# Kernel tuning notes

Hardware: AMD Instinct MI355X
Metric: run time of the kernel (lower is better)

The kernel has to match this reference:

```python
import jax, jax.numpy as jnp
import numpy as np

MOMENTUM = 0.9


def setup_inputs() -> dict:
    key = jax.random.key(0)
    k1, k2, k3, k4 = jax.random.split(key, 4)
    B, D, C = 524288, 256, 1000
    x = jax.random.normal(k1, (B, D), dtype=jnp.float32)
    l = jax.random.randint(k2, (B,), 0, C, dtype=jnp.int64)
    center_img = jax.random.normal(k3, (C, D), dtype=jnp.float32)
    center_skt = jax.random.normal(k4, (C, D), dtype=jnp.float32)
    return {"x": x, "l": l, "center_img": center_img, "center_skt": center_skt}


def reference(x, l, center_img, center_skt):
    # Faithful vectorized version of CenterAlignment.forward (modality='img').
    # The per-sample Python scatter-add loop -> segment_sum over fixed num_classes;
    # torch.unique's data-dependent class set -> boolean 'present' mask.
    C = center_img.shape[0]
    counts = jax.ops.segment_sum(jnp.ones(x.shape[0], dtype=x.dtype), l, num_segments=C)  # [C]
    sums = jax.ops.segment_sum(x, l, num_segments=C)                                      # [C, D]
    present = counts > 0
    mean = sums / jnp.maximum(counts, 1.0)[:, None]  # per-class mean (safe div for absent classes)
    # momentum update + L2 renormalization, only for classes present in the batch
    upd = center_img * MOMENTUM + mean * (1.0 - MOMENTUM)
    upd = upd / jnp.linalg.norm(upd, axis=1, keepdims=True)
    new_img = jnp.where(present[:, None], upd, center_img)
    # align_loss with alpha=2: mean over present classes of ||c_img - c_skt||^2
    diff = new_img - center_skt
    sq = jnp.sum(diff * diff, axis=1)  # [C]
    n_present = jnp.maximum(jnp.sum(present.astype(x.dtype)), 1.0)
    loss = jnp.sum(jnp.where(present, sq, 0.0)) / n_present
    return loss
```

## Files before the change

kernel.cpp:

```cpp
#include <hip/hip_runtime.h>

#define MAXC    1000
#define DSUB    16
#define LSTR    17
#define THREADS 1024
#define NCHUNK  32
#define FIXS    1048576.0f
#define INVFIXS (1.0f / 1048576.0f)

__global__ __launch_bounds__(THREADS, 8) void scatter_kernel(
    const float* __restrict__ x, const int* __restrict__ l,
    int* __restrict__ sums_i, int* __restrict__ cnt_i,
    int B, int D, int C, int chunk)
{
    __shared__ int lsum[MAXC * LSTR];
    __shared__ int lcnt[MAXC];

    for (int i = threadIdx.x; i < MAXC * LSTR; i += THREADS) lsum[i] = 0;
    for (int i = threadIdx.x; i < MAXC; i += THREADS) lcnt[i] = 0;
    __syncthreads();

    const bool doCount = (blockIdx.y == 0);
    const int dbase = blockIdx.y * DSUB;
    const int q    = threadIdx.x & 3;
    const int srel = threadIdx.x >> 2;
    const int STEP = THREADS >> 2;
    const int DV   = D >> 2;
    const int qb   = (dbase >> 2) + q;

    const float4* __restrict__ x4 = (const float4*)x;

    const int s0 = blockIdx.x * chunk;
    const int s1 = min(B, s0 + chunk);

#define ACC4(cc, vv)                                                   \
    {                                                                  \
        const int b_ = (cc) * LSTR + (q << 2);                         \
        atomicAdd(&lsum[b_ + 0], __float2int_rn((vv).x * FIXS));       \
        atomicAdd(&lsum[b_ + 1], __float2int_rn((vv).y * FIXS));       \
        atomicAdd(&lsum[b_ + 2], __float2int_rn((vv).z * FIXS));       \
        atomicAdd(&lsum[b_ + 3], __float2int_rn((vv).w * FIXS));       \
    }

    int s = s0 + srel;
    if (s + 3 * STEP < s1) {
        int c0 = l[s];
        int c1 = l[s + STEP];
        int c2 = l[s + 2 * STEP];
        int c3 = l[s + 3 * STEP];
        float4 v0 = x4[(size_t)s * DV + qb];
        float4 v1 = x4[(size_t)(s + STEP) * DV + qb];
        float4 v2 = x4[(size_t)(s + 2 * STEP) * DV + qb];
        float4 v3 = x4[(size_t)(s + 3 * STEP) * DV + qb];
        int sn = s + 4 * STEP;
        for (; sn + 3 * STEP < s1; sn += 4 * STEP) {
            int n0 = l[sn];
            int n1 = l[sn + STEP];
            int n2 = l[sn + 2 * STEP];
            int n3 = l[sn + 3 * STEP];
            float4 w0 = x4[(size_t)sn * DV + qb];
            float4 w1 = x4[(size_t)(sn + STEP) * DV + qb];
            float4 w2 = x4[(size_t)(sn + 2 * STEP) * DV + qb];
            float4 w3 = x4[(size_t)(sn + 3 * STEP) * DV + qb];
            ACC4(c0, v0); ACC4(c1, v1); ACC4(c2, v2); ACC4(c3, v3);
            if (doCount && q == 0) {
                atomicAdd(&lcnt[c0], 1);
                atomicAdd(&lcnt[c1], 1);
                atomicAdd(&lcnt[c2], 1);
                atomicAdd(&lcnt[c3], 1);
            }
            c0 = n0; c1 = n1; c2 = n2; c3 = n3;
            v0 = w0; v1 = w1; v2 = w2; v3 = w3;
        }
        ACC4(c0, v0); ACC4(c1, v1); ACC4(c2, v2); ACC4(c3, v3);
        if (doCount && q == 0) {
            atomicAdd(&lcnt[c0], 1);
            atomicAdd(&lcnt[c1], 1);
            atomicAdd(&lcnt[c2], 1);
            atomicAdd(&lcnt[c3], 1);
        }
        s = sn;
    }
    for (; s < s1; s += STEP) {
        int c = l[s];
        float4 v = x4[(size_t)s * DV + qb];
        ACC4(c, v);
        if (doCount && q == 0) atomicAdd(&lcnt[c], 1);
    }
    __syncthreads();

    for (int i = threadIdx.x; i < C * DSUB; i += THREADS) {
        const int c = i >> 4, d = i & (DSUB - 1);
        const int v = lsum[c * LSTR + d];
        if (v) atomicAdd(&sums_i[(size_t)c * D + dbase + d], v);
    }
    if (doCount)
        for (int i = threadIdx.x; i < C; i += THREADS) {
            const int v = lcnt[i];
            if (v) atomicAdd(&cnt_i[i], v);
        }
#undef ACC4
}

__device__ __forceinline__ float block_reduce_sum_256(float v, float* sbuf) {
    #pragma unroll
    for (int o = 32; o > 0; o >>= 1) v += __shfl_down(v, o, 64);
    __syncthreads();
    if ((threadIdx.x & 63) == 0) sbuf[threadIdx.x >> 6] = v;
    __syncthreads();
    return sbuf[0] + sbuf[1] + sbuf[2] + sbuf[3];
}

__global__ __launch_bounds__(256) void update_kernel(
    const int* __restrict__ sums_i, const int* __restrict__ cnt_i,
    const float* __restrict__ cimg, const float* __restrict__ cskt,
    float* __restrict__ sq_out, float* __restrict__ pres_out, int C, int D)
{
    __shared__ float sbuf[4];
    __shared__ float cshare;
    const int c = blockIdx.x;
    const int t = threadIdx.x;

    const float ssum = (float)sums_i[(size_t)c * D + t] * INVFIXS;
    if (t == 0) cshare = (float)cnt_i[c];
    __syncthreads();
    const float cnt = cshare;

    const bool present = cnt > 0.5f;
    const size_t idx = (size_t)c * D + t;
    const float ci = cimg[idx];
    const float cs = cskt[idx];
    const float mean = ssum / fmaxf(cnt, 1.f);
    const float upd = ci * 0.9f + mean * 0.1f;
    const float n2 = block_reduce_sum_256(upd * upd, sbuf);
    const float inv = 1.0f / sqrtf(n2);
    const float newv = present ? upd * inv : ci;
    const float df = newv - cs;
    const float sq = block_reduce_sum_256(df * df, sbuf);
    if (t == 0) {
        sq_out[c]   = present ? sq : 0.f;
        pres_out[c] = present ? 1.f : 0.f;
    }
}

__global__ __launch_bounds__(256) void finalize_kernel(
    const float* __restrict__ sq, const float* __restrict__ pres,
    float* __restrict__ out, int C)
{
    __shared__ float sbuf[4];
    float ls = 0.f, np = 0.f;
    for (int i = threadIdx.x; i < C; i += 256) {
        ls += sq[i];
        np += pres[i];
    }
    ls = block_reduce_sum_256(ls, sbuf);
    np = block_reduce_sum_256(np, sbuf);
    if (threadIdx.x == 0) out[0] = ls / fmaxf(np, 1.f);
}

extern "C" void kernel_launch(void* const* d_in, const int* in_sizes, int n_in,
                              void* d_out, int out_size, void* d_ws, size_t ws_size,
                              hipStream_t stream) {
    const float* x    = (const float*)d_in[0];
    const int*   l    = (const int*)d_in[1];
    const float* cimg = (const float*)d_in[2];
    const float* cskt = (const float*)d_in[3];

    const int B = in_sizes[1];
    const int D = in_sizes[0] / B;
    const int C = in_sizes[2] / D;

    int*   sums_i = (int*)d_ws;
    int*   cnt_i  = sums_i + (size_t)C * D;
    float* sq     = (float*)(cnt_i + C);
    float* pres   = sq + C;

    hipMemsetAsync(d_ws, 0, sizeof(int) * ((size_t)C * D + C), stream);

    const int chunk = (B + NCHUNK - 1) / NCHUNK;
    dim3 grid(NCHUNK, D / DSUB);

    scatter_kernel<<<grid, THREADS, 0, stream>>>(x, l, sums_i, cnt_i, B, D, C, chunk);
    update_kernel<<<C, 256, 0, stream>>>(sums_i, cnt_i, cimg, cskt, sq, pres, C, D);
    finalize_kernel<<<1, 256, 0, stream>>>(sq, pres, (float*)d_out, C);
}
```

Measured before the change: 142.4 us.

## Replace shared-memory atomic scatter with counting-sort by class then segmented sums

Replaces the per-block LDS-atomic scatter with a pipeline: histogram of labels, prefix scan, a permutation build that groups row indices by class, then a wave-per-span segmented sum that reads rows in sorted order and flushes register accumulators to global memory with atomics only at class boundaries. This is meant to remove the heavy LDS atomic traffic. In exchange it adds three extra launches, global atomics on per-class cursors, and gathered (non-contiguous) row reads of x. The build step also makes the within-class order nondeterministic, though the integer fixed-point sums stay exact.

Measured after the change: 168.7 us. 1.18x slower.

```diff
diff --git a/kernel.cpp b/kernel.cpp
--- a/kernel.cpp
+++ b/kernel.cpp
@@ -1,105 +1,109 @@
 #include <hip/hip_runtime.h>
 
-#define MAXC    1000
-#define DSUB    16
-#define LSTR    17
-#define THREADS 1024
-#define NCHUNK  32
+#define CMAX    1000
+#define CPAD    64
 #define FIXS    1048576.0f
 #define INVFIXS (1.0f / 1048576.0f)
 
-__global__ __launch_bounds__(THREADS, 8) void scatter_kernel(
-    const float* __restrict__ x, const int* __restrict__ l,
-    int* __restrict__ sums_i, int* __restrict__ cnt_i,
-    int B, int D, int C, int chunk)
+__global__ __launch_bounds__(256) void hist_kernel(
+    const int* __restrict__ l, int* __restrict__ tot, int B)
 {
-    __shared__ int lsum[MAXC * LSTR];
-    __shared__ int lcnt[MAXC];
+    __shared__ int h[CMAX];
+    for (int i = threadIdx.x; i < CMAX; i += 256) h[i] = 0;
+    __syncthreads();
+    const int per  = (B + gridDim.x - 1) / gridDim.x;
+    const int base = blockIdx.x * per;
+    const int end  = min(B, base + per);
+    for (int i = base + threadIdx.x; i < end; i += 256)
+        atomicAdd(&h[l[i]], 1);
+    __syncthreads();
+    for (int i = threadIdx.x; i < CMAX; i += 256) {
+        const int v = h[i];
+        if (v) atomicAdd(&tot[i], v);
+    }
+}
 
-    for (int i = threadIdx.x; i < MAXC * LSTR; i += THREADS) lsum[i] = 0;
-    for (int i = threadIdx.x; i < MAXC; i += THREADS) lcnt[i] = 0;
+__global__ __launch_bounds__(1024) void scan_kernel(
+    const int* __restrict__ tot, int* __restrict__ cursor,
+    int* __restrict__ cnt_i, int C)
+{
+    __shared__ int s[1024];
+    const int t = threadIdx.x;
+    const int v = (t < C) ? tot[t] : 0;
+    s[t] = v;
+    if (t < C) cnt_i[t] = v;
+    for (int off = 1; off < 1024; off <<= 1) {
+        __syncthreads();
+        const int u = (t >= off) ? s[t - off] : 0;
+        __syncthreads();
+        s[t] += u;
+    }
     __syncthreads();
+    if (t < C) cursor[t * CPAD] = s[t] - v;
+}
 
-    const bool doCount = (blockIdx.y == 0);
-    const int dbase = blockIdx.y * DSUB;
-    const int q    = threadIdx.x & 3;
-    const int srel = threadIdx.x >> 2;
-    const int STEP = THREADS >> 2;
-    const int DV   = D >> 2;
-    const int qb   = (dbase >> 2) + q;
+__global__ __launch_bounds__(256) void build_kernel(
+    const int* __restrict__ l, int* __restrict__ cursor,
+    int* __restrict__ perm, int* __restrict__ lsorted, int B)
+{
+    const int per  = (B + gridDim.x - 1) / gridDim.x;
+    const int base = blockIdx.x * per;
+    const int end  = min(B, base + per);
+    for (int i = base + threadIdx.x; i < end; i += 256) {
+        const int c   = l[i];
+        const int pos = atomicAdd(&cursor[c * CPAD], 1);
+        perm[pos]    = i;
+        lsorted[pos] = c;
+    }
+}
 
+#define SPAN 64
+__global__ __launch_bounds__(256) void segsum_kernel(
+    const float* __restrict__ x, const int* __restrict__ perm,
+    const int* __restrict__ lsorted, int* __restrict__ sums_i, int B, int D)
+{
+    const int lane = threadIdx.x & 63;
+    const int wid  = (int)((blockIdx.x * blockDim.x + threadIdx.x) >> 6);
+    const int p0 = wid * SPAN;
+    if (p0 >= B) return;
+    const int p1 = min(B, p0 + SPAN);
+    const int DV = D >> 2;
     const float4* __restrict__ x4 = (const float4*)x;
 
-    const int s0 = blockIdx.x * chunk;
-    const int s1 = min(B, s0 + chunk);
+    int cur = lsorted[p0];
+    int ax = 0, ay = 0, az = 0, aw = 0;
 
-#define ACC4(cc, vv)                                                   \
-    {                                                                  \
-        const int b_ = (cc) * LSTR + (q << 2);                         \
-        atomicAdd(&lsum[b_ + 0], __float2int_rn((vv).x * FIXS));       \
-        atomicAdd(&lsum[b_ + 1], __float2int_rn((vv).y * FIXS));       \
-        atomicAdd(&lsum[b_ + 2], __float2int_rn((vv).z * FIXS));       \
-        atomicAdd(&lsum[b_ + 3], __float2int_rn((vv).w * FIXS));       \
+    int    c_n   = cur;
+    int    idx_n = perm[p0];
+    float4 v_n   = x4[(size_t)idx_n * DV + lane];
+
+    for (int p = p0; p < p1; ++p) {
+        const float4 v = v_n;
+        const int    c = c_n;
+        if (p + 1 < p1) {
+            const int idx2 = perm[p + 1];
+            c_n = lsorted[p + 1];
+            v_n = x4[(size_t)idx2 * DV + lane];
+        }
+        if (c != cur) {
+            int* dst = sums_i + (size_t)cur * D + (lane << 2);
+            atomicAdd(dst + 0, ax);
+            atomicAdd(dst + 1, ay);
+            atomicAdd(dst + 2, az);
+            atomicAdd(dst + 3, aw);
+            ax = ay = az = aw = 0;
+            cur = c;
+        }
+        ax += __float2int_rn(v.x * FIXS);
+        ay += __float2int_rn(v.y * FIXS);
+        az += __float2int_rn(v.z * FIXS);
+        aw += __float2int_rn(v.w * FIXS);
     }
-
-    int s = s0 + srel;
-    if (s + 3 * STEP < s1) {
-        int c0 = l[s];
-        int c1 = l[s + STEP];
-        int c2 = l[s + 2 * STEP];
-        int c3 = l[s + 3 * STEP];
-        float4 v0 = x4[(size_t)s * DV + qb];
-        float4 v1 = x4[(size_t)(s + STEP) * DV + qb];
-        float4 v2 = x4[(size_t)(s + 2 * STEP) * DV + qb];
-        float4 v3 = x4[(size_t)(s + 3 * STEP) * DV + qb];
-        int sn = s + 4 * STEP;
-        for (; sn + 3 * STEP < s1; sn += 4 * STEP) {
-            int n0 = l[sn];
-            int n1 = l[sn + STEP];
-            int n2 = l[sn + 2 * STEP];
-            int n3 = l[sn + 3 * STEP];
-            float4 w0 = x4[(size_t)sn * DV + qb];
-            float4 w1 = x4[(size_t)(sn + STEP) * DV + qb];
-            float4 w2 = x4[(size_t)(sn + 2 * STEP) * DV + qb];
-            float4 w3 = x4[(size_t)(sn + 3 * STEP) * DV + qb];
-            ACC4(c0, v0); ACC4(c1, v1); ACC4(c2, v2); ACC4(c3, v3);
-            if (doCount && q == 0) {
-                atomicAdd(&lcnt[c0], 1);
-                atomicAdd(&lcnt[c1], 1);
-                atomicAdd(&lcnt[c2], 1);
-                atomicAdd(&lcnt[c3], 1);
-            }
-            c0 = n0; c1 = n1; c2 = n2; c3 = n3;
-            v0 = w0; v1 = w1; v2 = w2; v3 = w3;
-        }
-        ACC4(c0, v0); ACC4(c1, v1); ACC4(c2, v2); ACC4(c3, v3);
-        if (doCount && q == 0) {
-            atomicAdd(&lcnt[c0], 1);
-            atomicAdd(&lcnt[c1], 1);
-            atomicAdd(&lcnt[c2], 1);
-            atomicAdd(&lcnt[c3], 1);
-        }
-        s = sn;
-    }
-    for (; s < s1; s += STEP) {
-        int c = l[s];
-        float4 v = x4[(size_t)s * DV + qb];
-        ACC4(c, v);
-        if (doCount && q == 0) atomicAdd(&lcnt[c], 1);
-    }
-    __syncthreads();
-
-    for (int i = threadIdx.x; i < C * DSUB; i += THREADS) {
-        const int c = i >> 4, d = i & (DSUB - 1);
-        const int v = lsum[c * LSTR + d];
-        if (v) atomicAdd(&sums_i[(size_t)c * D + dbase + d], v);
-    }
-    if (doCount)
-        for (int i = threadIdx.x; i < C; i += THREADS) {
-            const int v = lcnt[i];
-            if (v) atomicAdd(&cnt_i[i], v);
-        }
-#undef ACC4
+    int* dst = sums_i + (size_t)cur * D + (lane << 2);
+    atomicAdd(dst + 0, ax);
+    atomicAdd(dst + 1, ay);
+    atomicAdd(dst + 2, az);
+    atomicAdd(dst + 3, aw);
 }
 
 __device__ __forceinline__ float block_reduce_sum_256(float v, float* sbuf) {
@@ -170,17 +174,26 @@
     const int D = in_sizes[0] / B;
     const int C = in_sizes[2] / D;
 
-    int*   sums_i = (int*)d_ws;
-    int*   cnt_i  = sums_i + (size_t)C * D;
-    float* sq     = (float*)(cnt_i + C);
+    int* ws_i     = (int*)d_ws;
+    int* sums_i   = ws_i;
+    int* tot      = sums_i + (size_t)C * D;
+    int* cnt_i    = tot + C;
+    int* cursor   = cnt_i + C;
+    int* perm     = cursor + (size_t)C * CPAD;
+    int* lsorted  = perm + B;
+    float* sq     = (float*)(lsorted + B);
     float* pres   = sq + C;
 
-    hipMemsetAsync(d_ws, 0, sizeof(int) * ((size_t)C * D + C), stream);
+    hipMemsetAsync(sums_i, 0, sizeof(int) * ((size_t)C * D + C), stream);
 
-    const int chunk = (B + NCHUNK - 1) / NCHUNK;
-    dim3 grid(NCHUNK, D / DSUB);
+    hist_kernel<<<256, 256, 0, stream>>>(l, tot, B);
+    scan_kernel<<<1, 1024, 0, stream>>>(tot, cursor, cnt_i, C);
+    build_kernel<<<256, 256, 0, stream>>>(l, cursor, perm, lsorted, B);
 
-    scatter_kernel<<<grid, THREADS, 0, stream>>>(x, l, sums_i, cnt_i, B, D, C, chunk);
+    const int rowsPerBlock = 4 * SPAN;
+    const int dblocks = (B + rowsPerBlock - 1) / rowsPerBlock;
+    segsum_kernel<<<dblocks, 256, 0, stream>>>(x, perm, lsorted, sums_i, B, D);
+
     update_kernel<<<C, 256, 0, stream>>>(sums_i, cnt_i, cimg, cskt, sq, pres, C, D);
     finalize_kernel<<<1, 256, 0, stream>>>(sq, pres, (float*)d_out, C);
 }
```

## Pack two biased fixed-point values into one 64-bit LDS atomic

Applied to the files above, without the earlier changes.

Each x value is biased by +8 and scaled by 2^16 to an unsigned 32-bit fixed-point number, and two of them are packed into one 64-bit shared-memory atomicAdd. This halves the number of LDS atomics in the scatter. The D slice per block doubles to 32, which halves the grid, and the load loop is unrolled to eight samples using float2 loads. The update kernel removes the bias in double precision. In exchange, fixed-point precision drops from 2^-20 to 2^-16, inputs outside the bias range give wrong sums, and the 128KB shared tile lowers occupancy to one block per CU.

Result: slower. 164.6 us (+15.5%).

```diff
diff --git a/kernel.cpp b/kernel.cpp
--- a/kernel.cpp
+++ b/kernel.cpp
@@ -1,105 +1,88 @@
 #include <hip/hip_runtime.h>
 
-#define MAXC    1000
-#define DSUB    16
-#define LSTR    17
+#define CMAX    1000
+#define DSUB    32
+#define W64     16
 #define THREADS 1024
 #define NCHUNK  32
-#define FIXS    1048576.0f
-#define INVFIXS (1.0f / 1048576.0f)
+#define BIAS    8.0f
+#define SCALE   65536.0f
 
-__global__ __launch_bounds__(THREADS, 8) void scatter_kernel(
+__global__ __launch_bounds__(THREADS) void scatter_kernel(
     const float* __restrict__ x, const int* __restrict__ l,
-    int* __restrict__ sums_i, int* __restrict__ cnt_i,
+    unsigned int* __restrict__ sums_u, unsigned int* __restrict__ cnt_u,
     int B, int D, int C, int chunk)
 {
-    __shared__ int lsum[MAXC * LSTR];
-    __shared__ int lcnt[MAXC];
+    __shared__ unsigned long long lsum[CMAX * W64];
+    __shared__ unsigned int      lcnt[CMAX];
 
-    for (int i = threadIdx.x; i < MAXC * LSTR; i += THREADS) lsum[i] = 0;
-    for (int i = threadIdx.x; i < MAXC; i += THREADS) lcnt[i] = 0;
+    for (int i = threadIdx.x; i < CMAX * W64; i += THREADS) lsum[i] = 0ULL;
+    for (int i = threadIdx.x; i < CMAX; i += THREADS) lcnt[i] = 0u;
     __syncthreads();
 
     const bool doCount = (blockIdx.y == 0);
     const int dbase = blockIdx.y * DSUB;
-    const int q    = threadIdx.x & 3;
-    const int srel = threadIdx.x >> 2;
-    const int STEP = THREADS >> 2;
-    const int DV   = D >> 2;
-    const int qb   = (dbase >> 2) + q;
+    const int w    = threadIdx.x & 15;
+    const int srel = threadIdx.x >> 4;
+    const int STEP = THREADS >> 4;
+    const int DV2  = D >> 1;
+    const int off2 = (dbase >> 1) + w;
 
-    const float4* __restrict__ x4 = (const float4*)x;
+    const float2* __restrict__ x2 = (const float2*)x;
 
     const int s0 = blockIdx.x * chunk;
     const int s1 = min(B, s0 + chunk);
 
-#define ACC4(cc, vv)                                                   \
-    {                                                                  \
-        const int b_ = (cc) * LSTR + (q << 2);                         \
-        atomicAdd(&lsum[b_ + 0], __float2int_rn((vv).x * FIXS));       \
-        atomicAdd(&lsum[b_ + 1], __float2int_rn((vv).y * FIXS));       \
-        atomicAdd(&lsum[b_ + 2], __float2int_rn((vv).z * FIXS));       \
-        atomicAdd(&lsum[b_ + 3], __float2int_rn((vv).w * FIXS));       \
-    }
-
     int s = s0 + srel;
-    if (s + 3 * STEP < s1) {
-        int c0 = l[s];
-        int c1 = l[s + STEP];
-        int c2 = l[s + 2 * STEP];
-        int c3 = l[s + 3 * STEP];
-        float4 v0 = x4[(size_t)s * DV + qb];
-        float4 v1 = x4[(size_t)(s + STEP) * DV + qb];
-        float4 v2 = x4[(size_t)(s + 2 * STEP) * DV + qb];
-        float4 v3 = x4[(size_t)(s + 3 * STEP) * DV + qb];
-        int sn = s + 4 * STEP;
-        for (; sn + 3 * STEP < s1; sn += 4 * STEP) {
-            int n0 = l[sn];
-            int n1 = l[sn + STEP];
-            int n2 = l[sn + 2 * STEP];
-            int n3 = l[sn + 3 * STEP];
-            float4 w0 = x4[(size_t)sn * DV + qb];
-            float4 w1 = x4[(size_t)(sn + STEP) * DV + qb];
-            float4 w2 = x4[(size_t)(sn + 2 * STEP) * DV + qb];
-            float4 w3 = x4[(size_t)(sn + 3 * STEP) * DV + qb];
-            ACC4(c0, v0); ACC4(c1, v1); ACC4(c2, v2); ACC4(c3, v3);
-            if (doCount && q == 0) {
-                atomicAdd(&lcnt[c0], 1);
-                atomicAdd(&lcnt[c1], 1);
-                atomicAdd(&lcnt[c2], 1);
-                atomicAdd(&lcnt[c3], 1);
-            }
-            c0 = n0; c1 = n1; c2 = n2; c3 = n3;
-            v0 = w0; v1 = w1; v2 = w2; v3 = w3;
+    for (; s + 7 * STEP < s1; s += 8 * STEP) {
+        int    cc[8];
+        float2 vv[8];
+        #pragma unroll
+        for (int k = 0; k < 8; ++k) {
+            const int sk = s + k * STEP;
+            cc[k] = l[sk];
+            vv[k] = x2[(size_t)sk * DV2 + off2];
         }
-        ACC4(c0, v0); ACC4(c1, v1); ACC4(c2, v2); ACC4(c3, v3);
-        if (doCount && q == 0) {
-            atomicAdd(&lcnt[c0], 1);
-            atomicAdd(&lcnt[c1], 1);
-            atomicAdd(&lcnt[c2], 1);
-            atomicAdd(&lcnt[c3], 1);
+        #pragma unroll
+        for (int k = 0; k < 8; ++k) {
+            const unsigned lo = __float2uint_rn((vv[k].x + BIAS) * SCALE);
+            const unsigned hi = __float2uint_rn((vv[k].y + BIAS) * SCALE);
+            const unsigned long long pk =
+                ((unsigned long long)hi << 32) | (unsigned long long)lo;
+            atomicAdd(&lsum[cc[k] * W64 + w], pk);
         }
-        s = sn;
+        if (doCount && w == 0) {
+            #pragma unroll
+            for (int k = 0; k < 8; ++k) atomicAdd(&lcnt[cc[k]], 1u);
+        }
     }
     for (; s < s1; s += STEP) {
-        int c = l[s];
-        float4 v = x4[(size_t)s * DV + qb];
-        ACC4(c, v);
-        if (doCount && q == 0) atomicAdd(&lcnt[c], 1);
+        const int c = l[s];
+        const float2 v = x2[(size_t)s * DV2 + off2];
+        const unsigned lo = __float2uint_rn((v.x + BIAS) * SCALE);
+        const unsigned hi = __float2uint_rn((v.y + BIAS) * SCALE);
+        atomicAdd(&lsum[c * W64 + w],
+                  ((unsigned long long)hi << 32) | (unsigned long long)lo);
+        if (doCount && w == 0) atomicAdd(&lcnt[c], 1u);
     }
     __syncthreads();
 
-    for (int i = threadIdx.x; i < C * DSUB; i += THREADS) {
-        const int c = i >> 4, d = i & (DSUB - 1);
-        const int v = lsum[c * LSTR + d];
-        if (v) atomicAdd(&sums_i[(size_t)c * D + dbase + d], v);
+    for (int i = threadIdx.x; i < C * W64; i += THREADS) {
+        const unsigned long long val = lsum[i];
+        if (val) {
+            const int c = i >> 4, ww = i & 15;
+            const unsigned lo = (unsigned)(val & 0xffffffffULL);
+            const unsigned hi = (unsigned)(val >> 32);
+            unsigned* dst = sums_u + (size_t)c * D + dbase + (ww << 1);
+            if (lo) atomicAdd(dst, lo);
+            if (hi) atomicAdd(dst + 1, hi);
+        }
     }
     if (doCount)
         for (int i = threadIdx.x; i < C; i += THREADS) {
-            const int v = lcnt[i];
-            if (v) atomicAdd(&cnt_i[i], v);
+            const unsigned v = lcnt[i];
+            if (v) atomicAdd(&cnt_u[i], v);
         }
-#undef ACC4
 }
 
 __device__ __forceinline__ float block_reduce_sum_256(float v, float* sbuf) {
@@ -112,7 +95,7 @@
 }
 
 __global__ __launch_bounds__(256) void update_kernel(
-    const int* __restrict__ sums_i, const int* __restrict__ cnt_i,
+    const unsigned int* __restrict__ sums_u, const unsigned int* __restrict__ cnt_u,
     const float* __restrict__ cimg, const float* __restrict__ cskt,
     float* __restrict__ sq_out, float* __restrict__ pres_out, int C, int D)
 {
@@ -121,16 +104,17 @@
     const int c = blockIdx.x;
     const int t = threadIdx.x;
 
-    const float ssum = (float)sums_i[(size_t)c * D + t] * INVFIXS;
-    if (t == 0) cshare = (float)cnt_i[c];
+    const unsigned su = sums_u[(size_t)c * D + t];
+    if (t == 0) cshare = (float)cnt_u[c];
     __syncthreads();
     const float cnt = cshare;
 
+    const double ssum = (double)su * (1.0 / 65536.0) - 8.0 * (double)cnt;
     const bool present = cnt > 0.5f;
     const size_t idx = (size_t)c * D + t;
     const float ci = cimg[idx];
     const float cs = cskt[idx];
-    const float mean = ssum / fmaxf(cnt, 1.f);
+    const float mean = (float)(ssum / (double)fmaxf(cnt, 1.f));
     const float upd = ci * 0.9f + mean * 0.1f;
     const float n2 = block_reduce_sum_256(upd * upd, sbuf);
     const float inv = 1.0f / sqrtf(n2);
@@ -170,17 +154,17 @@
     const int D = in_sizes[0] / B;
     const int C = in_sizes[2] / D;
 
-    int*   sums_i = (int*)d_ws;
-    int*   cnt_i  = sums_i + (size_t)C * D;
-    float* sq     = (float*)(cnt_i + C);
-    float* pres   = sq + C;
+    unsigned int* sums_u = (unsigned int*)d_ws;
+    unsigned int* cnt_u  = sums_u + (size_t)C * D;
+    float* sq            = (float*)(cnt_u + C);
+    float* pres          = sq + C;
 
-    hipMemsetAsync(d_ws, 0, sizeof(int) * ((size_t)C * D + C), stream);
+    hipMemsetAsync(d_ws, 0, sizeof(unsigned int) * ((size_t)C * D + C), stream);
 
     const int chunk = (B + NCHUNK - 1) / NCHUNK;
     dim3 grid(NCHUNK, D / DSUB);
 
-    scatter_kernel<<<grid, THREADS, 0, stream>>>(x, l, sums_i, cnt_i, B, D, C, chunk);
-    update_kernel<<<C, 256, 0, stream>>>(sums_i, cnt_i, cimg, cskt, sq, pres, C, D);
+    scatter_kernel<<<grid, THREADS, 0, stream>>>(x, l, sums_u, cnt_u, B, D, C, chunk);
+    update_kernel<<<C, 256, 0, stream>>>(sums_u, cnt_u, cimg, cskt, sq, pres, C, D);
     finalize_kernel<<<1, 256, 0, stream>>>(sq, pres, (float*)d_out, C);
 }
```
